# Optimization experiments

Hardware: AMD Instinct MI355X
Metric: run time of the kernel (lower is better)

The kernel has to match this reference:

```python
import jax, jax.numpy as jnp
import numpy as np

N_NODES = 100000
N_EDGES = 1600000
IN_F = 128
OUT_F = 128
EDGE_F = 16


def setup_inputs() -> dict:
    key = jax.random.key(0)
    ks = jax.random.split(key, 8)
    H = jax.random.normal(ks[0], (N_NODES, IN_F), dtype=jnp.float32)
    edge_index = jax.random.randint(ks[1], (2, N_EDGES), 0, N_ODES_ := N_NODES, dtype=jnp.int64) if False else jax.random.randint(ks[1], (2, N_EDGES), 0, N_NODES, dtype=jnp.int32).astype(jnp.int64)
    edge_attr = jax.random.normal(ks[2], (N_EDGES, EDGE_F), dtype=jnp.float32)
    We = jax.random.normal(ks[3], (EDGE_F, IN_F), dtype=jnp.float32) * (1.0 / np.sqrt(EDGE_F))
    be = jnp.zeros((IN_F,), dtype=jnp.float32)
    W1 = jax.random.normal(ks[4], (IN_F, OUT_F), dtype=jnp.float32) * (1.0 / np.sqrt(IN_F))
    b1 = jnp.zeros((OUT_F,), dtype=jnp.float32)
    W2 = jax.random.normal(ks[5], (OUT_F, OUT_F), dtype=jnp.float32) * (1.0 / np.sqrt(OUT_F))
    b2 = jnp.zeros((OUT_F,), dtype=jnp.float32)
    return {"H": H, "edge_index": edge_index, "edge_attr": edge_attr,
            "We": We, "be": be, "W1": W1, "b1": b1, "W2": W2, "b2": b2}


def reference(H, edge_index, edge_attr, We, be, W1, b1, W2, b2):
    # edge_mlp: Linear(edge_attr_dim -> in_features)
    edge_messages = edge_attr @ We + be                       # [E, in_f]
    # gather by src, add edge messages
    messages = H[edge_index[0]] + edge_messages               # [E, in_f]
    # scatter_add by dst with dim_size = N
    aggregated = jax.ops.segment_sum(messages, edge_index[1], num_segments=H.shape[0])  # [N, in_f]
    # node_mlp: Linear -> ReLU -> Linear
    h = jax.nn.relu(aggregated @ W1 + b1)                     # [N, out_f]
    out = h @ W2 + b2                                         # [N, out_f]
    return out
```

## Files before the change

### kernel.cpp

```cpp
#include <hip/hip_runtime.h>

#define IN_F 128
#define EF 16

typedef short bf16x8 __attribute__((ext_vector_type(8)));
typedef float f32x4  __attribute__((ext_vector_type(4)));

__device__ __forceinline__ unsigned short f2b(float f) {
    unsigned b = __float_as_uint(f);
    b += 0x7fffu + ((b >> 16) & 1u);
    return (unsigned short)(b >> 16);
}
__device__ __forceinline__ float blo(unsigned u) { return __uint_as_float(u << 16); }
__device__ __forceinline__ float bhi(unsigned u) { return __uint_as_float(u & 0xffff0000u); }


__global__ __launch_bounds__(256) void pre_kernel(
    const float* __restrict__ H, unsigned short* __restrict__ Hb, int n4,
    const int* __restrict__ ei, int* __restrict__ counts,
    int* __restrict__ rank, int E,
    const float* __restrict__ W1, unsigned short* __restrict__ W1t,
    const float* __restrict__ W2, unsigned short* __restrict__ W2t,
    const float* __restrict__ EA, float* __restrict__ aggE,
    int h2b_blocks, int hist_blocks)
{
    int b = blockIdx.x;
    if (b < h2b_blocks) {
        int i = b * 256 + threadIdx.x;
        if (i < n4) {
            float4 v = ((const float4*)H)[i];
            ushort4 r;
            r.x = f2b(v.x); r.y = f2b(v.y); r.z = f2b(v.z); r.w = f2b(v.w);
            ((ushort4*)Hb)[i] = r;
        }
    } else if (b < h2b_blocks + hist_blocks) {
        int e = (b - h2b_blocks) * 256 + threadIdx.x;
        if (e < E) rank[e] = atomicAdd(&counts[ei[E + e]], 1);
    } else if (b < h2b_blocks + hist_blocks + 128) {
        int idx = (b - h2b_blocks - hist_blocks) * 256 + threadIdx.x;
        int w = idx >> 14;
        int r = idx & 16383;
        int n = r >> 7, k = r & 127;
        if (w == 0) W1t[n * IN_F + k] = f2b(W1[k * IN_F + n]);
        else        W2t[n * IN_F + k] = f2b(W2[k * IN_F + n]);
    } else {
        long long idx = (long long)(b - h2b_blocks - hist_blocks - 128) * 256 + threadIdx.x;
        if (idx < (long long)E * EF) {
            int e = (int)(idx >> 4);
            int f = (int)(idx & 15);
            int dst = ei[E + e];
            atomicAdd(&aggE[dst * EF + f], EA[idx]);
        }
    }
}

__global__ __launch_bounds__(256) void hist_kernel(
    const int* __restrict__ ei, int* __restrict__ counts,
    int* __restrict__ rank, int E)
{
    int e = blockIdx.x * 256 + threadIdx.x;
    if (e >= E) return;
    rank[e] = atomicAdd(&counts[ei[E + e]], 1);
}

__global__ __launch_bounds__(256) void scan_blocks_kernel(
    const int* __restrict__ in, int* __restrict__ out,
    int* __restrict__ partials, int n)
{
    __shared__ int sdata[256];
    const int t = threadIdx.x;
    const int idx0 = blockIdx.x * 1024 + t * 4;
    int v[4];
    #pragma unroll
    for (int i = 0; i < 4; i++) { int idx = idx0 + i; v[i] = (idx < n) ? in[idx] : 0; }
    int s = v[0] + v[1] + v[2] + v[3];
    sdata[t] = s;
    __syncthreads();
    for (int off = 1; off < 256; off <<= 1) {
        int x = (t >= off) ? sdata[t - off] : 0;
        __syncthreads();
        sdata[t] += x;
        __syncthreads();
    }
    if (t == 255) partials[blockIdx.x] = sdata[255];
    int run = (t > 0) ? sdata[t - 1] : 0;
    #pragma unroll
    for (int i = 0; i < 4; i++) {
        int idx = idx0 + i;
        if (idx < n) out[idx] = run;
        run += v[i];
    }
}

__global__ __launch_bounds__(256) void scan_add_fused_kernel(
    int* __restrict__ out, const int* __restrict__ partials, int n)
{
    __shared__ int sw[4];
    const int t = threadIdx.x;
    const int g = blockIdx.x >> 2;
    int v = 0;
    for (int j = t; j < g; j += 256) v += partials[j];
    #pragma unroll
    for (int off = 1; off < 64; off <<= 1) v += __shfl_xor(v, off, 64);
    if ((t & 63) == 0) sw[t >> 6] = v;
    __syncthreads();
    int P = sw[0] + sw[1] + sw[2] + sw[3];
    int idx = blockIdx.x * 256 + t;
    if (idx < n) out[idx] += P;
}

__global__ __launch_bounds__(256) void build_src_kernel(
    const int* __restrict__ ei,
    const int* __restrict__ offsets, const int* __restrict__ rank,
    int* __restrict__ sorted_src, int E)
{
    int e = blockIdx.x * 256 + threadIdx.x;
    if (e >= E) return;
    int dst = ei[E + e];
    int pos = offsets[dst] + rank[e];
    sorted_src[pos] = ei[e];
}

__global__ __launch_bounds__(256) void build_kernel(
    const int* __restrict__ ei, int2* __restrict__ sorted,
    const int* __restrict__ offsets, const int* __restrict__ rank, int E)
{
    int e = blockIdx.x * 256 + threadIdx.x;
    if (e >= E) return;
    int src = ei[e];
    int dst = ei[E + e];
    int pos = offsets[dst] + rank[e];
    sorted[pos] = make_int2(src, e);
}

__global__ __launch_bounds__(256) void gather_agg_kernel(
    const unsigned short* __restrict__ Hb,
    const int* __restrict__ sorted_src,
    const int* __restrict__ offsets,
    const float* __restrict__ aggE,
    const float* __restrict__ We,
    const float* __restrict__ be,
    unsigned short* __restrict__ Ab,
    int N)
{
    int n = blockIdx.x * 4 + (threadIdx.x >> 6);
    if (n >= N) return;
    int lane = threadIdx.x & 63;
    int half = lane >> 5;
    int l32  = lane & 31;
    int s = offsets[n];
    int e_end = offsets[n + 1];
    float a0 = 0.f, a1 = 0.f, a2 = 0.f, a3 = 0.f;
    int i = s + half;
    for (; i + 6 < e_end; i += 8) {
        int s0 = sorted_src[i];
        int s1 = sorted_src[i + 2];
        int s2 = sorted_src[i + 4];
        int s3 = sorted_src[i + 6];
        uint2 u0 = *(const uint2*)(Hb + (long long)s0 * IN_F + l32 * 4);
        uint2 u1 = *(const uint2*)(Hb + (long long)s1 * IN_F + l32 * 4);
        uint2 u2 = *(const uint2*)(Hb + (long long)s2 * IN_F + l32 * 4);
        uint2 u3 = *(const uint2*)(Hb + (long long)s3 * IN_F + l32 * 4);
        a0 += (blo(u0.x) + blo(u1.x)) + (blo(u2.x) + blo(u3.x));
        a1 += (bhi(u0.x) + bhi(u1.x)) + (bhi(u2.x) + bhi(u3.x));
        a2 += (blo(u0.y) + blo(u1.y)) + (blo(u2.y) + blo(u3.y));
        a3 += (bhi(u0.y) + bhi(u1.y)) + (bhi(u2.y) + bhi(u3.y));
    }
    for (; i < e_end; i += 2) {
        int se = sorted_src[i];
        uint2 u = *(const uint2*)(Hb + (long long)se * IN_F + l32 * 4);
        a0 += blo(u.x); a1 += bhi(u.x); a2 += blo(u.y); a3 += bhi(u.y);
    }
    a0 += __shfl_xor(a0, 32, 64);
    a1 += __shfl_xor(a1, 32, 64);
    a2 += __shfl_xor(a2, 32, 64);
    a3 += __shfl_xor(a3, 32, 64);

    const int c4 = l32 * 4;
    const float deg = (float)(e_end - s);
    float4 bev = *(const float4*)&be[c4];
    float vx = a0 + deg * bev.x;
    float vy = a1 + deg * bev.y;
    float vz = a2 + deg * bev.z;
    float vw = a3 + deg * bev.w;
    #pragma unroll
    for (int k = 0; k < EF; k++) {
        float ak = aggE[n * EF + k];
        float4 w = *(const float4*)&We[k * IN_F + c4];
        vx += ak * w.x; vy += ak * w.y; vz += ak * w.z; vw += ak * w.w;
    }
    if (half == 0) {
        ushort4 o;
        o.x = f2b(vx); o.y = f2b(vy); o.z = f2b(vz); o.w = f2b(vw);
        *(ushort4*)&Ab[(long long)n * IN_F + c4] = o;
    }
}

__global__ __launch_bounds__(256) void gather_f32_kernel(
    const float* __restrict__ H,
    const float* __restrict__ EA,
    const int2* __restrict__ sorted,
    const int* __restrict__ offsets,
    float* __restrict__ agg,
    float* __restrict__ aggE,
    float* __restrict__ degf,
    int N)
{
    int n = blockIdx.x * 4 + (threadIdx.x >> 6);
    if (n >= N) return;
    int lane = threadIdx.x & 63;
    int half = lane >> 5;
    int l32  = lane & 31;
    int s = offsets[n];
    int e_end = offsets[n + 1];
    float4 acc = make_float4(0.f, 0.f, 0.f, 0.f);
    float accE = 0.f;
    int i = s + half;
    for (; i + 6 < e_end; i += 8) {
        int2 s0 = sorted[i];
        int2 s1 = sorted[i + 2];
        int2 s2 = sorted[i + 4];
        int2 s3 = sorted[i + 6];
        float4 v0 = *(const float4*)(H + (long long)s0.x * IN_F + l32 * 4);
        float4 v1 = *(const float4*)(H + (long long)s1.x * IN_F + l32 * 4);
        float4 v2 = *(const float4*)(H + (long long)s2.x * IN_F + l32 * 4);
        float4 v3 = *(const float4*)(H + (long long)s3.x * IN_F + l32 * 4);
        float e0 = 0.f, e1 = 0.f, e2 = 0.f, e3 = 0.f;
        if (l32 < EF) {
            e0 = EA[(long long)s0.y * EF + l32];
            e1 = EA[(long long)s1.y * EF + l32];
            e2 = EA[(long long)s2.y * EF + l32];
            e3 = EA[(long long)s3.y * EF + l32];
        }
        acc.x += (v0.x + v1.x) + (v2.x + v3.x);
        acc.y += (v0.y + v1.y) + (v2.y + v3.y);
        acc.z += (v0.z + v1.z) + (v2.z + v3.z);
        acc.w += (v0.w + v1.w) + (v2.w + v3.w);
        accE  += (e0 + e1) + (e2 + e3);
    }
    for (; i < e_end; i += 2) {
        int2 se = sorted[i];
        float4 v = *(const float4*)(H + (long long)se.x * IN_F + l32 * 4);
        acc.x += v.x; acc.y += v.y; acc.z += v.z; acc.w += v.w;
        if (l32 < EF) accE += EA[(long long)se.y * EF + l32];
    }
    acc.x += __shfl_xor(acc.x, 32, 64);
    acc.y += __shfl_xor(acc.y, 32, 64);
    acc.z += __shfl_xor(acc.z, 32, 64);
    acc.w += __shfl_xor(acc.w, 32, 64);
    accE  += __shfl_xor(accE, 32, 64);
    if (half == 0) {
        *(float4*)(agg + (long long)n * IN_F + l32 * 4) = acc;
        if (l32 < EF) aggE[n * EF + l32] = accE;
        if (l32 == 0) degf[n] = (float)(e_end - s);
    }
}

__global__ __launch_bounds__(256) void edge_scatter_kernel(
    const float* __restrict__ H,
    const int* __restrict__ ei,
    const float* __restrict__ EA,
    float* __restrict__ agg,
    float* __restrict__ aggE,
    float* __restrict__ deg,
    int E)
{
    long long gid = (long long)blockIdx.x * 256 + threadIdx.x;
    int e = (int)(gid >> 7);
    if (e >= E) return;
    int f = (int)(gid & 127);
    int src = ei[e];
    int dst = ei[E + e];
    float m = H[(long long)src * IN_F + f];
    atomicAdd(&agg[(long long)dst * IN_F + f], m);
    if (f < EF) atomicAdd(&aggE[dst * EF + f], EA[e * EF + f]);
    if (f == 0) atomicAdd(&deg[dst], 1.0f);
}


#define XPITCH 136
__global__ __launch_bounds__(256) void mlp_mfma_kernel(
    const unsigned short* __restrict__ Ab,
    const unsigned short* __restrict__ W1t,
    const unsigned short* __restrict__ W2t,
    const float* __restrict__ b1, const float* __restrict__ b2,
    float* __restrict__ out, int N)
{
    __shared__ unsigned short sW[128 * XPITCH];
    __shared__ unsigned short sX[64 * XPITCH];
    const int t    = threadIdx.x;
    const int tile = blockIdx.x * 64;
    const int lane = t & 63;
    const int wv   = t >> 6;
    const int quad = lane >> 4;
    const int lr   = lane & 15;
    const int M0   = wv * 16;

    {
        const uint4 z = make_uint4(0, 0, 0, 0);
        #pragma unroll
        for (int j = 0; j < 4; j++) {
            int idx = t + 256 * j;
            int row = idx >> 4, c = idx & 15;
            uint4 v = z;
            if (tile + row < N) v = ((const uint4*)Ab)[(long long)(tile + row) * 16 + c];
            ((uint4*)sX)[row * 17 + c] = v;
        }
        #pragma unroll
        for (int j = 0; j < 8; j++) {
            int idx = t + 256 * j;
            int row = idx >> 4, c = idx & 15;
            ((uint4*)sW)[row * 17 + c] = ((const uint4*)W1t)[idx];
        }
    }
    __syncthreads();

    f32x4 acc[8];
    bf16x8 af[4];
    const f32x4 zero = {0.f, 0.f, 0.f, 0.f};

    #pragma unroll
    for (int kt = 0; kt < 4; kt++)
        af[kt] = *(const bf16x8*)&sX[(M0 + lr) * XPITCH + kt * 32 + quad * 8];
    #pragma unroll
    for (int nt = 0; nt < 8; nt++) {
        acc[nt] = zero;
        #pragma unroll
        for (int kt = 0; kt < 4; kt++) {
            bf16x8 bf = *(const bf16x8*)&sW[(nt * 16 + lr) * XPITCH + kt * 32 + quad * 8];
            acc[nt] = __builtin_amdgcn_mfma_f32_16x16x32_bf16(af[kt], bf, acc[nt], 0, 0, 0);
        }
    }
    #pragma unroll
    for (int nt = 0; nt < 8; nt++) {
        int col = nt * 16 + lr;
        float bias = b1[col];
        #pragma unroll
        for (int r = 0; r < 4; r++) {
            float v = fmaxf(acc[nt][r] + bias, 0.f);
            sX[(M0 + quad * 4 + r) * XPITCH + col] = f2b(v);
        }
    }
    __syncthreads();
    #pragma unroll
    for (int j = 0; j < 8; j++) {
        int idx = t + 256 * j;
        int row = idx >> 4, c = idx & 15;
        ((uint4*)sW)[row * 17 + c] = ((const uint4*)W2t)[idx];
    }
    __syncthreads();

    #pragma unroll
    for (int kt = 0; kt < 4; kt++)
        af[kt] = *(const bf16x8*)&sX[(M0 + lr) * XPITCH + kt * 32 + quad * 8];
    #pragma unroll
    for (int nt = 0; nt < 8; nt++) {
        acc[nt] = zero;
        #pragma unroll
        for (int kt = 0; kt < 4; kt++) {
            bf16x8 bf = *(const bf16x8*)&sW[(nt * 16 + lr) * XPITCH + kt * 32 + quad * 8];
            acc[nt] = __builtin_amdgcn_mfma_f32_16x16x32_bf16(af[kt], bf, acc[nt], 0, 0, 0);
        }
    }
    #pragma unroll
    for (int nt = 0; nt < 8; nt++) {
        int col = nt * 16 + lr;
        float bias = b2[col];
        #pragma unroll
        for (int r = 0; r < 4; r++) {
            int row = tile + M0 + quad * 4 + r;
            if (row < N) out[(long long)row * IN_F + col] = acc[nt][r] + bias;
        }
    }
}

__global__ __launch_bounds__(256) void node_mlp_kernel(
    float* agg_out,
    const float* __restrict__ aggE,
    const float* __restrict__ degf,
    const float* __restrict__ We, const float* __restrict__ be,
    const float* __restrict__ W1, const float* __restrict__ b1,
    const float* __restrict__ W2, const float* __restrict__ b2,
    int N)
{
    __shared__ float sA[32][IN_F];
    __shared__ float sH[32][IN_F];
    const int t  = threadIdx.x;
    const int c4 = (t & 31) * 4;
    const int r0 = t >> 5;

    const int tile = blockIdx.x * 32;
    if (tile >= N) return;
    int rows = N - tile;
    if (rows > 32) rows = 32;

    {
        const float4 bev = *(const float4*)&be[c4];
        #pragma unroll
        for (int i = 0; i < 4; i++) {
            int rr = r0 + 8 * i;
            float4 v = make_float4(0.f, 0.f, 0.f, 0.f);
            if (rr < rows) {
                long long r = tile + rr;
                v = *(const float4*)&agg_out[r * IN_F + c4];
                float d = degf[r];
                v.x += d * bev.x; v.y += d * bev.y; v.z += d * bev.z; v.w += d * bev.w;
                #pragma unroll
                for (int k = 0; k < EF; k++) {
                    float a = aggE[r * EF + k];
                    float4 w = *(const float4*)&We[k * IN_F + c4];
                    v.x += a * w.x; v.y += a * w.y; v.z += a * w.z; v.w += a * w.w;
                }
            }
            *(float4*)&sA[rr][c4] = v;
        }
    }
    __syncthreads();
    {
        const float4 bv = *(const float4*)&b1[c4];
        float4 a0 = bv, a1 = bv, a2 = bv, a3 = bv;
        for (int k = 0; k < IN_F; k++) {
            float4 w = *(const float4*)&W1[k * IN_F + c4];
            float x0 = sA[r0][k], x1 = sA[r0 + 8][k], x2 = sA[r0 + 16][k], x3 = sA[r0 + 24][k];
            a0.x += x0 * w.x; a0.y += x0 * w.y; a0.z += x0 * w.z; a0.w += x0 * w.w;
            a1.x += x1 * w.x; a1.y += x1 * w.y; a1.z += x1 * w.z; a1.w += x1 * w.w;
            a2.x += x2 * w.x; a2.y += x2 * w.y; a2.z += x2 * w.z; a2.w += x2 * w.w;
            a3.x += x3 * w.x; a3.y += x3 * w.y; a3.z += x3 * w.z; a3.w += x3 * w.w;
        }
        a0.x = fmaxf(a0.x, 0.f); a0.y = fmaxf(a0.y, 0.f); a0.z = fmaxf(a0.z, 0.f); a0.w = fmaxf(a0.w, 0.f);
        a1.x = fmaxf(a1.x, 0.f); a1.y = fmaxf(a1.y, 0.f); a1.z = fmaxf(a1.z, 0.f); a1.w = fmaxf(a1.w, 0.f);
        a2.x = fmaxf(a2.x, 0.f); a2.y = fmaxf(a2.y, 0.f); a2.z = fmaxf(a2.z, 0.f); a2.w = fmaxf(a2.w, 0.f);
        a3.x = fmaxf(a3.x, 0.f); a3.y = fmaxf(a3.y, 0.f); a3.z = fmaxf(a3.z, 0.f); a3.w = fmaxf(a3.w, 0.f);
        *(float4*)&sH[r0][c4]      = a0;
        *(float4*)&sH[r0 + 8][c4]  = a1;
        *(float4*)&sH[r0 + 16][c4] = a2;
        *(float4*)&sH[r0 + 24][c4] = a3;
    }
    __syncthreads();
    {
        const float4 bv = *(const float4*)&b2[c4];
        float4 a0 = bv, a1 = bv, a2 = bv, a3 = bv;
        for (int k = 0; k < IN_F; k++) {
            float4 w = *(const float4*)&W2[k * IN_F + c4];
            float x0 = sH[r0][k], x1 = sH[r0 + 8][k], x2 = sH[r0 + 16][k], x3 = sH[r0 + 24][k];
            a0.x += x0 * w.x; a0.y += x0 * w.y; a0.z += x0 * w.z; a0.w += x0 * w.w;
            a1.x += x1 * w.x; a1.y += x1 * w.y; a1.z += x1 * w.z; a1.w += x1 * w.w;
            a2.x += x2 * w.x; a2.y += x2 * w.y; a2.z += x2 * w.z; a2.w += x2 * w.w;
            a3.x += x3 * w.x; a3.y += x3 * w.y; a3.z += x3 * w.z; a3.w += x3 * w.w;
        }
        #pragma unroll
        for (int i = 0; i < 4; i++) {
            int rr = r0 + 8 * i;
            if (rr < rows) {
                float4 v = (i == 0) ? a0 : (i == 1) ? a1 : (i == 2) ? a2 : a3;
                *(float4*)&agg_out[(long long)(tile + rr) * IN_F + c4] = v;
            }
        }
    }
}

extern "C" void kernel_launch(void* const* d_in, const int* in_sizes, int n_in,
                              void* d_out, int out_size, void* d_ws, size_t ws_size,
                              hipStream_t stream) {
    const float* H  = (const float*)d_in[0];
    const int*   ei = (const int*)d_in[1];
    const float* EA = (const float*)d_in[2];
    const float* We = (const float*)d_in[3];
    const float* be = (const float*)d_in[4];
    const float* W1 = (const float*)d_in[5];
    const float* b1 = (const float*)d_in[6];
    const float* W2 = (const float*)d_in[7];
    const float* b2 = (const float*)d_in[8];
    float* out = (float*)d_out;

    const int N = in_sizes[0] / IN_F;
    const int E = in_sizes[2] / EF;

    char* p = (char*)d_ws;
    auto alloc = [&](size_t bytes) { char* r = p; p += (bytes + 255) & ~(size_t)255; return r; };
    int2*  sorted   = (int2*)alloc((size_t)E * sizeof(int2));
    int*   sorted_src = (int*)sorted;
    int*   rank     = (int*)alloc((size_t)E * sizeof(int));
    float* degf     = (float*)alloc((size_t)N * sizeof(float));
    float* aggE     = (float*)alloc((size_t)N * EF * sizeof(float));
    int*   counts   = (int*)alloc((size_t)(N + 1) * sizeof(int));
    int*   offsets  = (int*)alloc((size_t)(N + 1) * sizeof(int));
    int*   partials = (int*)alloc(1024 * sizeof(int));
    size_t need_base = (size_t)(p - (char*)d_ws);
    unsigned short* Hb = (unsigned short*)alloc((size_t)N * IN_F * sizeof(unsigned short));
    unsigned short* Ab  = (unsigned short*)alloc((size_t)N * IN_F * sizeof(unsigned short));
    unsigned short* W1t = (unsigned short*)alloc((size_t)IN_F * IN_F * sizeof(unsigned short));
    unsigned short* W2t = (unsigned short*)alloc((size_t)IN_F * IN_F * sizeof(unsigned short));
    size_t need_mfma = (size_t)(p - (char*)d_ws);

    const int n_scan = N + 1;
    const int B = (n_scan + 1023) / 1024;
    const size_t zero_bytes = (size_t)((char*)offsets - (char*)aggE);

    if (ws_size >= need_mfma && B <= 1024) {
        hipMemsetAsync(aggE, 0, zero_bytes, stream);
        const int n4 = N * IN_F / 4;
        const int h2b_blocks  = (n4 + 255) / 256;
        const int hist_blocks = (E + 255) / 256;
        const long long ea_items = (long long)E * EF;
        const int ea_blocks = (int)((ea_items + 255) / 256);
        pre_kernel<<<h2b_blocks + hist_blocks + 128 + ea_blocks, 256, 0, stream>>>(
            H, Hb, n4, ei, counts, rank, E, W1, W1t, W2, W2t, EA, aggE,
            h2b_blocks, hist_blocks);
        scan_blocks_kernel<<<B, 256, 0, stream>>>(counts, offsets, partials, n_scan);
        scan_add_fused_kernel<<<(n_scan + 255) / 256, 256, 0, stream>>>(offsets, partials, n_scan);
        build_src_kernel<<<(E + 255) / 256, 256, 0, stream>>>(ei, offsets, rank, sorted_src, E);
        gather_agg_kernel<<<(N + 3) / 4, 256, 0, stream>>>(
            Hb, sorted_src, offsets, aggE, We, be, Ab, N);
        mlp_mfma_kernel<<<(N + 63) / 64, 256, 0, stream>>>(Ab, W1t, W2t, b1, b2, out, N);
    } else if (ws_size >= need_base && B <= 1024) {
        hipMemsetAsync(counts, 0, (size_t)(N + 1) * sizeof(int), stream);
        hist_kernel<<<(E + 255) / 256, 256, 0, stream>>>(ei, counts, rank, E);
        scan_blocks_kernel<<<B, 256, 0, stream>>>(counts, offsets, partials, n_scan);
        scan_add_fused_kernel<<<(n_scan + 255) / 256, 256, 0, stream>>>(offsets, partials, n_scan);
        build_kernel<<<(E + 255) / 256, 256, 0, stream>>>(ei, sorted, offsets, rank, E);
        gather_f32_kernel<<<(N + 3) / 4, 256, 0, stream>>>(H, EA, sorted, offsets, out, aggE, degf, N);
        node_mlp_kernel<<<(N + 31) / 32, 256, 0, stream>>>(out, aggE, degf, We, be, W1, b1, W2, b2, N);
    } else {
        float* f_aggE = (float*)d_ws;
        float* f_deg  = f_aggE + (size_t)N * EF;
        hipMemsetAsync(d_out, 0, (size_t)N * IN_F * sizeof(float), stream);
        hipMemsetAsync(d_ws, 0, (size_t)N * (EF + 1) * sizeof(float), stream);
        long long tot = (long long)E * IN_F;
        edge_scatter_kernel<<<(int)((tot + 255) / 256), 256, 0, stream>>>(H, ei, EA, out, f_aggE, f_deg, E);
        node_mlp_kernel<<<(N + 31) / 32, 256, 0, stream>>>(out, f_aggE, f_deg, We, be, W1, b1, W2, b2, N);
    }
}
```

Before: 498.9 us.

## Replace atomic edge-attr scatter with CSR-sorted per-node reduction kernel

Removes the 25.6M float atomicAdds that scattered edge attributes into aggE. Instead, build stores (src, edge id) pairs in dst-sorted CSR order, and a new ea_reduce_kernel gathers each node's edge attributes without atomics and writes aggE directly. The cost is a larger sorted array (int2 instead of int), an extra kernel launch, and random 64-byte reads of edge attribute rows. The gather kernel also reads strided int2 entries instead of packed ints.

```diff
diff --git a/kernel.cpp b/kernel.cpp
--- a/kernel.cpp
+++ b/kernel.cpp
@@ -21,7 +21,6 @@
     int* __restrict__ rank, int E,
     const float* __restrict__ W1, unsigned short* __restrict__ W1t,
     const float* __restrict__ W2, unsigned short* __restrict__ W2t,
-    const float* __restrict__ EA, float* __restrict__ aggE,
     int h2b_blocks, int hist_blocks)
 {
     int b = blockIdx.x;
@@ -36,21 +35,13 @@
     } else if (b < h2b_blocks + hist_blocks) {
         int e = (b - h2b_blocks) * 256 + threadIdx.x;
         if (e < E) rank[e] = atomicAdd(&counts[ei[E + e]], 1);
-    } else if (b < h2b_blocks + hist_blocks + 128) {
+    } else {
         int idx = (b - h2b_blocks - hist_blocks) * 256 + threadIdx.x;
         int w = idx >> 14;
         int r = idx & 16383;
         int n = r >> 7, k = r & 127;
         if (w == 0) W1t[n * IN_F + k] = f2b(W1[k * IN_F + n]);
         else        W2t[n * IN_F + k] = f2b(W2[k * IN_F + n]);
-    } else {
-        long long idx = (long long)(b - h2b_blocks - hist_blocks - 128) * 256 + threadIdx.x;
-        if (idx < (long long)E * EF) {
-            int e = (int)(idx >> 4);
-            int f = (int)(idx & 15);
-            int dst = ei[E + e];
-            atomicAdd(&aggE[dst * EF + f], EA[idx]);
-        }
     }
 }
 
@@ -107,18 +98,6 @@
     int P = sw[0] + sw[1] + sw[2] + sw[3];
     int idx = blockIdx.x * 256 + t;
     if (idx < n) out[idx] += P;
-}
-
-__global__ __launch_bounds__(256) void build_src_kernel(
-    const int* __restrict__ ei,
-    const int* __restrict__ offsets, const int* __restrict__ rank,
-    int* __restrict__ sorted_src, int E)
-{
-    int e = blockIdx.x * 256 + threadIdx.x;
-    if (e >= E) return;
-    int dst = ei[E + e];
-    int pos = offsets[dst] + rank[e];
-    sorted_src[pos] = ei[e];
 }
 
 __global__ __launch_bounds__(256) void build_kernel(
@@ -133,9 +112,41 @@
     sorted[pos] = make_int2(src, e);
 }
 
+__global__ __launch_bounds__(256) void ea_reduce_kernel(
+    const float* __restrict__ EA,
+    const int2* __restrict__ sorted,
+    const int* __restrict__ offsets,
+    float* __restrict__ aggE,
+    int N)
+{
+    int n = blockIdx.x * 4 + (threadIdx.x >> 6);
+    if (n >= N) return;
+    int lane = threadIdx.x & 63;
+    int sub  = lane >> 4;
+    int f    = lane & 15;
+    int s = offsets[n];
+    int e_end = offsets[n + 1];
+    float acc = 0.f;
+    int i = s + sub;
+    for (; i + 4 < e_end; i += 8) {
+        int e0 = sorted[i].y;
+        int e1 = sorted[i + 4].y;
+        float v0 = EA[(long long)e0 * EF + f];
+        float v1 = EA[(long long)e1 * EF + f];
+        acc += v0 + v1;
+    }
+    for (; i < e_end; i += 4) {
+        int e0 = sorted[i].y;
+        acc += EA[(long long)e0 * EF + f];
+    }
+    acc += __shfl_xor(acc, 16, 64);
+    acc += __shfl_xor(acc, 32, 64);
+    if (sub == 0) aggE[n * EF + f] = acc;
+}
+
 __global__ __launch_bounds__(256) void gather_agg_kernel(
     const unsigned short* __restrict__ Hb,
-    const int* __restrict__ sorted_src,
+    const int2* __restrict__ sorted,
     const int* __restrict__ offsets,
     const float* __restrict__ aggE,
     const float* __restrict__ We,
@@ -153,10 +164,10 @@
     float a0 = 0.f, a1 = 0.f, a2 = 0.f, a3 = 0.f;
     int i = s + half;
     for (; i + 6 < e_end; i += 8) {
-        int s0 = sorted_src[i];
-        int s1 = sorted_src[i + 2];
-        int s2 = sorted_src[i + 4];
-        int s3 = sorted_src[i + 6];
+        int s0 = sorted[i].x;
+        int s1 = sorted[i + 2].x;
+        int s2 = sorted[i + 4].x;
+        int s3 = sorted[i + 6].x;
         uint2 u0 = *(const uint2*)(Hb + (long long)s0 * IN_F + l32 * 4);
         uint2 u1 = *(const uint2*)(Hb + (long long)s1 * IN_F + l32 * 4);
         uint2 u2 = *(const uint2*)(Hb + (long long)s2 * IN_F + l32 * 4);
@@ -167,7 +178,7 @@
         a3 += (bhi(u0.y) + bhi(u1.y)) + (bhi(u2.y) + bhi(u3.y));
     }
     for (; i < e_end; i += 2) {
-        int se = sorted_src[i];
+        int se = sorted[i].x;
         uint2 u = *(const uint2*)(Hb + (long long)se * IN_F + l32 * 4);
         a0 += blo(u.x); a1 += bhi(u.x); a2 += blo(u.y); a3 += bhi(u.y);
     }
@@ -479,7 +490,6 @@
     char* p = (char*)d_ws;
     auto alloc = [&](size_t bytes) { char* r = p; p += (bytes + 255) & ~(size_t)255; return r; };
     int2*  sorted   = (int2*)alloc((size_t)E * sizeof(int2));
-    int*   sorted_src = (int*)sorted;
     int*   rank     = (int*)alloc((size_t)E * sizeof(int));
     float* degf     = (float*)alloc((size_t)N * sizeof(float));
     float* aggE     = (float*)alloc((size_t)N * EF * sizeof(float));
@@ -495,23 +505,20 @@
 
     const int n_scan = N + 1;
     const int B = (n_scan + 1023) / 1024;
-    const size_t zero_bytes = (size_t)((char*)offsets - (char*)aggE);
 
     if (ws_size >= need_mfma && B <= 1024) {
-        hipMemsetAsync(aggE, 0, zero_bytes, stream);
+        hipMemsetAsync(counts, 0, (size_t)(N + 1) * sizeof(int), stream);
         const int n4 = N * IN_F / 4;
         const int h2b_blocks  = (n4 + 255) / 256;
         const int hist_blocks = (E + 255) / 256;
-        const long long ea_items = (long long)E * EF;
-        const int ea_blocks = (int)((ea_items + 255) / 256);
-        pre_kernel<<<h2b_blocks + hist_blocks + 128 + ea_blocks, 256, 0, stream>>>(
-            H, Hb, n4, ei, counts, rank, E, W1, W1t, W2, W2t, EA, aggE,
-            h2b_blocks, hist_blocks);
+        pre_kernel<<<h2b_blocks + hist_blocks + 128, 256, 0, stream>>>(
+            H, Hb, n4, ei, counts, rank, E, W1, W1t, W2, W2t, h2b_blocks, hist_blocks);
         scan_blocks_kernel<<<B, 256, 0, stream>>>(counts, offsets, partials, n_scan);
         scan_add_fused_kernel<<<(n_scan + 255) / 256, 256, 0, stream>>>(offsets, partials, n_scan);
-        build_src_kernel<<<(E + 255) / 256, 256, 0, stream>>>(ei, offsets, rank, sorted_src, E);
+        build_kernel<<<(E + 255) / 256, 256, 0, stream>>>(ei, sorted, offsets, rank, E);
+        ea_reduce_kernel<<<(N + 3) / 4, 256, 0, stream>>>(EA, sorted, offsets, aggE, N);
         gather_agg_kernel<<<(N + 3) / 4, 256, 0, stream>>>(
-            Hb, sorted_src, offsets, aggE, We, be, Ab, N);
+            Hb, sorted, offsets, aggE, We, be, Ab, N);
         mlp_mfma_kernel<<<(N + 63) / 64, 256, 0, stream>>>(Ab, W1t, W2t, b1, b2, out, N);
     } else if (ws_size >= need_base && B <= 1024) {
         hipMemsetAsync(counts, 0, (size_t)(N + 1) * sizeof(int), stream);
```

New measurement: 491.8 us. Within noise of the previous version (-1.4%).
